# Kernel tuning notes

Measured on AMD Instinct MI355X. Metric: run time of the kernel, lower is better.

## Reference

```python
import jax, jax.numpy as jnp
import numpy as np


def setup_inputs() -> dict:
    key = jax.random.key(0)
    k1, k2 = jax.random.split(key)
    B, K, D = 65536, 4096, 64
    x = jax.random.normal(k1, (B, D), dtype=jnp.float32)
    nodes = jax.random.normal(k2, (K, D), dtype=jnp.float32)  # self.nodes parameter
    return {"x": x, "nodes": nodes}


def reference(x, nodes):
    # torch.cdist(x, nodes, p=2): Euclidean distance matrix [B, K]
    x2 = jnp.sum(x * x, axis=-1, keepdims=True)            # [B, 1]
    n2 = jnp.sum(nodes * nodes, axis=-1)[None, :]          # [1, K]
    d2 = x2 + n2 - 2.0 * (x @ nodes.T)                     # [B, K]
    distances = jnp.sqrt(jnp.maximum(d2, 0.0))
    winning_indices = jnp.argmin(distances, axis=-1)       # [B]
    node_repr = nodes[winning_indices]                     # [B, D] gather
    return node_repr, winning_indices
```

## Files before the change

kernel.cpp:

```cpp
#include <hip/hip_runtime.h>
#include <stdint.h>


typedef unsigned short u16;
typedef __bf16 bf16x8 __attribute__((ext_vector_type(8)));
typedef unsigned short u16x8 __attribute__((ext_vector_type(8)));
typedef float f32x16 __attribute__((ext_vector_type(16)));

#define B_ROWS 65536
#define K_NODES 4096
#define DIM 64
#define CSHIFT 300.0f
#define MERGE_TAU 0.012f

#define OFF_LIST 64
#define OFF_N2F  262208
#define OFF_N2D  278592
#define OFF_BFRAG 311360

__device__ __forceinline__ u16 bf16_rne(float f, float& back) {
    uint32_t u = __float_as_uint(f);
    uint32_t r = u + 0x7FFFu + ((u >> 16) & 1u);
    u16 h = (u16)(r >> 16);
    back = __uint_as_float(((uint32_t)h) << 16);
    return h;
}

__device__ __forceinline__ float pack_tile6(float v, uint32_t t) {
    return __uint_as_float((__float_as_uint(v) & 0xFFFFFFC0u) | t);
}

__global__ __launch_bounds__(256) void prep(const float* __restrict__ nodes,
                                            u16* __restrict__ bfrag,
                                            float* __restrict__ hn2f,
                                            double* __restrict__ n2d,
                                            int* __restrict__ ref_cnt) {
    if (blockIdx.x < 128) {
        int idx = blockIdx.x * 256 + threadIdx.x;
        int t = idx >> 8;
        int rem = idx & 255;
        int l = rem >> 2, c = rem & 3;
        const float* row = nodes + (size_t)(t * 32 + (l & 31)) * DIM + ((l >> 5) * 8);
        float4 f0 = *(const float4*)(row + c * 16);
        float4 f1 = *(const float4*)(row + c * 16 + 4);
        float fs[8] = {-f0.x, -f0.y, -f0.z, -f0.w, -f1.x, -f1.y, -f1.z, -f1.w};
        u16x8 hv, lv;
        #pragma unroll
        for (int j = 0; j < 8; ++j) {
            float hf, dummy;
            u16 hb = bf16_rne(fs[j], hf);
            u16 lb = bf16_rne(fs[j] - hf, dummy);
            hv[j] = hb; lv[j] = lb;
        }
        int base = ((t * 4 + c) * 2) * 512 + l * 8;
        *(u16x8*)(bfrag + base)       = hv;
        *(u16x8*)(bfrag + base + 512) = lv;
    } else {
        if (blockIdx.x == 128 && threadIdx.x == 0) *ref_cnt = 0;
        int k = (blockIdx.x - 128) * 256 + threadIdx.x;
        if (k < K_NODES) {
            const float* r = nodes + (size_t)k * DIM;
            double s = 0.0;
            #pragma unroll
            for (int d = 0; d < DIM; ++d) { double v = (double)r[d]; s += v * v; }
            n2d[k] = s;
            hn2f[k] = CSHIFT + 0.5f * (float)s;
        }
    }
}

__global__ __launch_bounds__(256, 2) void phase1(const float* __restrict__ x,
                                                 const u16* __restrict__ bfrag_g,
                                                 const float* __restrict__ hn2f,
                                                 float* __restrict__ out) {
    const int tid  = threadIdx.x;
    const int lane = tid & 63;
    const int w    = tid >> 6;
    const int col  = lane & 31;
    const int lh   = lane >> 5;
    const int rb   = blockIdx.x >> 1;
    const int h    = blockIdx.x & 1;
    const int rbase = rb * 256 + w * 64;

    bf16x8 ah[2][4], al[2][4];
    #pragma unroll
    for (int t = 0; t < 2; ++t) {
        const float* xp = x + (size_t)(rbase + t * 32 + col) * DIM + lh * 8;
        #pragma unroll
        for (int c = 0; c < 4; ++c) {
            float4 f0 = *(const float4*)(xp + c * 16);
            float4 f1 = *(const float4*)(xp + c * 16 + 4);
            float fs[8] = {f0.x, f0.y, f0.z, f0.w, f1.x, f1.y, f1.z, f1.w};
            u16x8 hv, lv;
            #pragma unroll
            for (int j = 0; j < 8; ++j) {
                float hf, dummy;
                u16 hb = bf16_rne(fs[j], hf);
                u16 lb = bf16_rne(fs[j] - hf, dummy);
                hv[j] = hb; lv[j] = lb;
            }
            union { u16x8 u; bf16x8 b; } cvh, cvl;
            cvh.u = hv; cvl.u = lv;
            ah[t][c] = cvh.b; al[t][c] = cvl.b;
        }
    }

    float b1[2][16], v2[2][16];
    #pragma unroll
    for (int t = 0; t < 2; ++t)
        #pragma unroll
        for (int q = 0; q < 16; ++q) { b1[t][q] = 3.4e38f; v2[t][q] = 3.4e38f; }

    const char* qbase = (const char*)bfrag_g + (size_t)h * 524288 + (size_t)lane * 16;
    const float* hp = hn2f + h * 2048 + col;

    bf16x8 h0, l0, h1, l1, h2, l2, h3, l3;

    #define LD(dsth, dstl, tt, cc) do {                                         \
        const char* _p = qbase + (size_t)(tt) * 8192 + (cc) * 2048;             \
        dsth = *(const bf16x8*)(_p);                                            \
        dstl = *(const bf16x8*)(_p + 1024);                                     \
    } while (0)

    #define MF6(B_h, B_l, cc) do {                                              \
        a0 = __builtin_amdgcn_mfma_f32_32x32x16_bf16(ah[0][cc], B_h, a0, 0, 0, 0); \
        a1 = __builtin_amdgcn_mfma_f32_32x32x16_bf16(ah[1][cc], B_h, a1, 0, 0, 0); \
        a0 = __builtin_amdgcn_mfma_f32_32x32x16_bf16(al[0][cc], B_h, a0, 0, 0, 0); \
        a1 = __builtin_amdgcn_mfma_f32_32x32x16_bf16(al[1][cc], B_h, a1, 0, 0, 0); \
        a0 = __builtin_amdgcn_mfma_f32_32x32x16_bf16(ah[0][cc], B_l, a0, 0, 0, 0); \
        a1 = __builtin_amdgcn_mfma_f32_32x32x16_bf16(ah[1][cc], B_l, a1, 0, 0, 0); \
    } while (0)

    LD(h0, l0, 0, 0);
    LD(h1, l1, 0, 1);
    float hn2_cur = hp[0];

    for (int t = 0; t < 64; ++t) {
        const int tn = (t + 1 < 64) ? t + 1 : 63;
        float hn2_nxt = hp[tn * 32];
        f32x16 a0, a1;
        #pragma unroll
        for (int q = 0; q < 16; ++q) { a0[q] = hn2_cur; a1[q] = hn2_cur; }

        LD(h2, l2, t, 2);
        MF6(h0, l0, 0);
        LD(h3, l3, t, 3);
        MF6(h1, l1, 1);
        LD(h0, l0, tn, 0);
        MF6(h2, l2, 2);
        LD(h1, l1, tn, 1);
        MF6(h3, l3, 3);

        const uint32_t tb = (uint32_t)t;
        #pragma unroll
        for (int q = 0; q < 16; ++q) {
            float p0 = pack_tile6(a0[q], tb);
            v2[0][q] = fminf(v2[0][q], fmaxf(p0, b1[0][q]));
            b1[0][q] = fminf(b1[0][q], p0);
            float p1 = pack_tile6(a1[q], tb);
            v2[1][q] = fminf(v2[1][q], fmaxf(p1, b1[1][q]));
            b1[1][q] = fminf(b1[1][q], p1);
        }
        hn2_cur = hn2_nxt;
    }
    #undef LD
    #undef MF6

    int gi[2][16];
    #pragma unroll
    for (int t = 0; t < 2; ++t)
        #pragma unroll
        for (int q = 0; q < 16; ++q)
            gi[t][q] = (int)(__float_as_uint(b1[t][q]) & 63u) * 32 + col;

    #pragma unroll
    for (int off = 1; off < 32; off <<= 1) {
        #pragma unroll
        for (int t = 0; t < 2; ++t)
            #pragma unroll
            for (int q = 0; q < 16; ++q) {
                float ov  = __shfl_xor(b1[t][q], off, 64);
                float ov2 = __shfl_xor(v2[t][q], off, 64);
                int   og  = __shfl_xor(gi[t][q], off, 64);
                float hi2 = fmaxf(b1[t][q], ov);
                v2[t][q] = fminf(fminf(v2[t][q], ov2), hi2);
                bool take = (ov < b1[t][q]) || (ov == b1[t][q] && og < gi[t][q]);
                b1[t][q] = take ? ov : b1[t][q];
                gi[t][q] = take ? og : gi[t][q];
            }
    }

    if (col == 0) {
        #pragma unroll
        for (int t = 0; t < 2; ++t)
            #pragma unroll
            for (int q = 0; q < 16; ++q) {
                int rloc = (q & 3) + 8 * (q >> 2) + 4 * lh;
                int grow = rb * 256 + w * 64 + t * 32 + rloc;
                float v2p = __uint_as_float((__float_as_uint(v2[t][q]) & 0xFFFFFFE0u)
                                            | (uint32_t)(gi[t][q] & 31));
                *(float2*)(out + (size_t)grow * DIM + h * 2) = make_float2(b1[t][q], v2p);
            }
    }
}

__global__ __launch_bounds__(256) void merge_k(const float* __restrict__ nodes,
                                               float* __restrict__ out,
                                               int* __restrict__ ref_cnt,
                                               int* __restrict__ ref_list) {
    __shared__ int s_win[256];
    const int tid = threadIdx.x;
    const int row = blockIdx.x * 256 + tid;
    float4 cv = *(const float4*)(out + (size_t)row * DIM);
    bool h1w = cv.z < cv.x;
    float wb = h1w ? cv.z : cv.x;
    float lb = h1w ? cv.x : cv.z;
    float v2m = fminf(fminf(cv.y, cv.w), lb);
    uint32_t wbits = __float_as_uint(wb);
    uint32_t vp    = __float_as_uint(h1w ? cv.w : cv.y);
    int gi = (h1w ? 2048 : 0) + (int)(wbits & 63u) * 32 + (int)(vp & 31u);
    out[(size_t)B_ROWS * DIM + row] = (float)gi;
    if (v2m - wb <= MERGE_TAU) {
        int slot = atomicAdd(ref_cnt, 1);
        ref_list[slot] = row;
    }
    s_win[tid] = gi;
    __syncthreads();
    const int base_row = blockIdx.x * 256;
    for (int i = tid; i < 256 * 16; i += 256) {
        int rr = i >> 4, cc = i & 15;
        int wn = s_win[rr];
        float4 v = *(const float4*)(nodes + (size_t)wn * DIM + cc * 4);
        *(float4*)(out + (size_t)(base_row + rr) * DIM + cc * 4) = v;
    }
}

__global__ __launch_bounds__(256) void phase2(const float* __restrict__ x,
                                              const float* __restrict__ nodes,
                                              const double* __restrict__ n2d,
                                              const int* __restrict__ ref_cnt,
                                              const int* __restrict__ ref_list,
                                              float* __restrict__ out) {
    __shared__ double xs[DIM];
    __shared__ double sval[256];
    __shared__ int    sidx[256];
    const int cnt = *ref_cnt;
    for (int li = blockIdx.x; li < cnt; li += gridDim.x) {
        const int row = ref_list[li];
        __syncthreads();
        if (threadIdx.x < DIM) xs[threadIdx.x] = (double)x[(size_t)row * DIM + threadIdx.x];
        __syncthreads();
        double best = 1e300; int bidx = K_NODES;
        for (int k = threadIdx.x; k < K_NODES; k += 256) {
            const float4* np4 = (const float4*)(nodes + (size_t)k * DIM);
            double d0 = 0.0, d1 = 0.0;
            #pragma unroll
            for (int t = 0; t < 16; t += 2) {
                float4 w0 = np4[t], w1 = np4[t + 1];
                d0 += xs[t*4+0]*(double)w0.x + xs[t*4+1]*(double)w0.y
                    + xs[t*4+2]*(double)w0.z + xs[t*4+3]*(double)w0.w;
                d1 += xs[t*4+4]*(double)w1.x + xs[t*4+5]*(double)w1.y
                    + xs[t*4+6]*(double)w1.z + xs[t*4+7]*(double)w1.w;
            }
            double s = n2d[k] - 2.0 * (d0 + d1);
            if (s < best) { best = s; bidx = k; }
        }
        sval[threadIdx.x] = best; sidx[threadIdx.x] = bidx;
        __syncthreads();
        for (int stride = 128; stride > 0; stride >>= 1) {
            if (threadIdx.x < (unsigned)stride) {
                double ov = sval[threadIdx.x + stride];
                int    oi = sidx[threadIdx.x + stride];
                if (ov < sval[threadIdx.x] ||
                    (ov == sval[threadIdx.x] && oi < sidx[threadIdx.x])) {
                    sval[threadIdx.x] = ov; sidx[threadIdx.x] = oi;
                }
            }
            __syncthreads();
        }
        const int wn = sidx[0];
        if (threadIdx.x == 0) out[(size_t)B_ROWS * DIM + row] = (float)wn;
        if (threadIdx.x < 16) {
            float4 v = *(const float4*)(nodes + (size_t)wn * DIM + threadIdx.x * 4);
            *(float4*)(out + (size_t)row * DIM + threadIdx.x * 4) = v;
        }
        __syncthreads();
    }
}

extern "C" void kernel_launch(void* const* d_in, const int* in_sizes, int n_in,
                              void* d_out, int out_size, void* d_ws, size_t ws_size,
                              hipStream_t stream) {
    const float* x     = (const float*)d_in[0];
    const float* nodes = (const float*)d_in[1];
    float* out = (float*)d_out;
    char*  ws  = (char*)d_ws;

    int*    ref_cnt  = (int*)ws;
    int*    ref_list = (int*)(ws + OFF_LIST);
    float*  hn2f     = (float*)(ws + OFF_N2F);
    double* n2d      = (double*)(ws + OFF_N2D);
    u16*    bfrag    = (u16*)(ws + OFF_BFRAG);

    prep<<<144, 256, 0, stream>>>(nodes, bfrag, hn2f, n2d, ref_cnt);
    phase1<<<512, 256, 0, stream>>>(x, bfrag, hn2f, out);
    merge_k<<<B_ROWS / 256, 256, 0, stream>>>(nodes, out, ref_cnt, ref_list);
    phase2<<<1024, 256, 0, stream>>>(x, nodes, n2d, ref_cnt, ref_list, out);
}
```

Before: 205.6 us.

## Split node range into four quarters per block and shrink per-wave row tile

Phase1 now gives each wave 32 rows instead of 64 and splits the 4096 nodes into four quarters of 1024 across blocks, launching 2048 blocks instead of 512. Per-thread accumulators and register state are halved, which is meant to raise occupancy and parallelism, at the cost of reloading node fragments more often per row and doing more cross-lane reductions. The tile index tag shrinks to 5 bits, merge combines four partial results instead of two, and the refinement threshold is lowered so fewer rows go to the exact fp64 pass, which trades some safety margin for less phase2 work.

```diff
diff --git a/kernel.cpp b/kernel.cpp
--- a/kernel.cpp
+++ b/kernel.cpp
@@ -11,7 +11,7 @@
 #define K_NODES 4096
 #define DIM 64
 #define CSHIFT 300.0f
-#define MERGE_TAU 0.012f
+#define MERGE_TAU 0.009f
 
 #define OFF_LIST 64
 #define OFF_N2F  262208
@@ -26,8 +26,8 @@
     return h;
 }
 
-__device__ __forceinline__ float pack_tile6(float v, uint32_t t) {
-    return __uint_as_float((__float_as_uint(v) & 0xFFFFFFC0u) | t);
+__device__ __forceinline__ float pack_tile5(float v, uint32_t t) {
+    return __uint_as_float((__float_as_uint(v) & 0xFFFFFFE0u) | t);
 }
 
 __global__ __launch_bounds__(256) void prep(const float* __restrict__ nodes,
@@ -78,14 +78,13 @@
     const int w    = tid >> 6;
     const int col  = lane & 31;
     const int lh   = lane >> 5;
-    const int rb   = blockIdx.x >> 1;
-    const int h    = blockIdx.x & 1;
-    const int rbase = rb * 256 + w * 64;
-
-    bf16x8 ah[2][4], al[2][4];
-    #pragma unroll
-    for (int t = 0; t < 2; ++t) {
-        const float* xp = x + (size_t)(rbase + t * 32 + col) * DIM + lh * 8;
+    const int rb   = blockIdx.x >> 2;
+    const int qid  = blockIdx.x & 3;
+    const int rbase = rb * 128 + w * 32;
+
+    bf16x8 ah[4], al[4];
+    {
+        const float* xp = x + (size_t)(rbase + col) * DIM + lh * 8;
         #pragma unroll
         for (int c = 0; c < 4; ++c) {
             float4 f0 = *(const float4*)(xp + c * 16);
@@ -101,18 +100,16 @@
             }
             union { u16x8 u; bf16x8 b; } cvh, cvl;
             cvh.u = hv; cvl.u = lv;
-            ah[t][c] = cvh.b; al[t][c] = cvl.b;
-        }
-    }
-
-    float b1[2][16], v2[2][16];
+            ah[c] = cvh.b; al[c] = cvl.b;
+        }
+    }
+
+    float b1[16], v2[16];
     #pragma unroll
-    for (int t = 0; t < 2; ++t)
-        #pragma unroll
-        for (int q = 0; q < 16; ++q) { b1[t][q] = 3.4e38f; v2[t][q] = 3.4e38f; }
-
-    const char* qbase = (const char*)bfrag_g + (size_t)h * 524288 + (size_t)lane * 16;
-    const float* hp = hn2f + h * 2048 + col;
+    for (int q = 0; q < 16; ++q) { b1[q] = 3.4e38f; v2[q] = 3.4e38f; }
+
+    const char* qbase = (const char*)bfrag_g + (size_t)qid * 262144 + (size_t)lane * 16;
+    const float* hp = hn2f + qid * 1024 + col;
 
     bf16x8 h0, l0, h1, l1, h2, l2, h3, l3;
 
@@ -122,85 +119,73 @@
         dstl = *(const bf16x8*)(_p + 1024);                                     \
     } while (0)
 
-    #define MF6(B_h, B_l, cc) do {                                              \
-        a0 = __builtin_amdgcn_mfma_f32_32x32x16_bf16(ah[0][cc], B_h, a0, 0, 0, 0); \
-        a1 = __builtin_amdgcn_mfma_f32_32x32x16_bf16(ah[1][cc], B_h, a1, 0, 0, 0); \
-        a0 = __builtin_amdgcn_mfma_f32_32x32x16_bf16(al[0][cc], B_h, a0, 0, 0, 0); \
-        a1 = __builtin_amdgcn_mfma_f32_32x32x16_bf16(al[1][cc], B_h, a1, 0, 0, 0); \
-        a0 = __builtin_amdgcn_mfma_f32_32x32x16_bf16(ah[0][cc], B_l, a0, 0, 0, 0); \
-        a1 = __builtin_amdgcn_mfma_f32_32x32x16_bf16(ah[1][cc], B_l, a1, 0, 0, 0); \
+    #define MF3(B_h, B_l, cc) do {                                              \
+        a0 = __builtin_amdgcn_mfma_f32_32x32x16_bf16(ah[cc], B_h, a0, 0, 0, 0); \
+        a0 = __builtin_amdgcn_mfma_f32_32x32x16_bf16(al[cc], B_h, a0, 0, 0, 0); \
+        a0 = __builtin_amdgcn_mfma_f32_32x32x16_bf16(ah[cc], B_l, a0, 0, 0, 0); \
     } while (0)
 
     LD(h0, l0, 0, 0);
     LD(h1, l1, 0, 1);
     float hn2_cur = hp[0];
 
-    for (int t = 0; t < 64; ++t) {
-        const int tn = (t + 1 < 64) ? t + 1 : 63;
+    for (int t = 0; t < 32; ++t) {
+        const int tn = (t + 1 < 32) ? t + 1 : 31;
         float hn2_nxt = hp[tn * 32];
-        f32x16 a0, a1;
-        #pragma unroll
-        for (int q = 0; q < 16; ++q) { a0[q] = hn2_cur; a1[q] = hn2_cur; }
+        f32x16 a0;
+        #pragma unroll
+        for (int q = 0; q < 16; ++q) a0[q] = hn2_cur;
 
         LD(h2, l2, t, 2);
-        MF6(h0, l0, 0);
+        MF3(h0, l0, 0);
         LD(h3, l3, t, 3);
-        MF6(h1, l1, 1);
+        MF3(h1, l1, 1);
         LD(h0, l0, tn, 0);
-        MF6(h2, l2, 2);
+        MF3(h2, l2, 2);
         LD(h1, l1, tn, 1);
-        MF6(h3, l3, 3);
+        MF3(h3, l3, 3);
 
         const uint32_t tb = (uint32_t)t;
         #pragma unroll
         for (int q = 0; q < 16; ++q) {
-            float p0 = pack_tile6(a0[q], tb);
-            v2[0][q] = fminf(v2[0][q], fmaxf(p0, b1[0][q]));
-            b1[0][q] = fminf(b1[0][q], p0);
-            float p1 = pack_tile6(a1[q], tb);
-            v2[1][q] = fminf(v2[1][q], fmaxf(p1, b1[1][q]));
-            b1[1][q] = fminf(b1[1][q], p1);
+            float p0 = pack_tile5(a0[q], tb);
+            v2[q] = fminf(v2[q], fmaxf(p0, b1[q]));
+            b1[q] = fminf(b1[q], p0);
         }
         hn2_cur = hn2_nxt;
     }
     #undef LD
-    #undef MF6
-
-    int gi[2][16];
+    #undef MF3
+
+    int gi[16];
     #pragma unroll
-    for (int t = 0; t < 2; ++t)
-        #pragma unroll
-        for (int q = 0; q < 16; ++q)
-            gi[t][q] = (int)(__float_as_uint(b1[t][q]) & 63u) * 32 + col;
+    for (int q = 0; q < 16; ++q)
+        gi[q] = (int)(__float_as_uint(b1[q]) & 31u) * 32 + col;
 
     #pragma unroll
     for (int off = 1; off < 32; off <<= 1) {
         #pragma unroll
-        for (int t = 0; t < 2; ++t)
-            #pragma unroll
-            for (int q = 0; q < 16; ++q) {
-                float ov  = __shfl_xor(b1[t][q], off, 64);
-                float ov2 = __shfl_xor(v2[t][q], off, 64);
-                int   og  = __shfl_xor(gi[t][q], off, 64);
-                float hi2 = fmaxf(b1[t][q], ov);
-                v2[t][q] = fminf(fminf(v2[t][q], ov2), hi2);
-                bool take = (ov < b1[t][q]) || (ov == b1[t][q] && og < gi[t][q]);
-                b1[t][q] = take ? ov : b1[t][q];
-                gi[t][q] = take ? og : gi[t][q];
-            }
+        for (int q = 0; q < 16; ++q) {
+            float ov  = __shfl_xor(b1[q], off, 64);
+            float ov2 = __shfl_xor(v2[q], off, 64);
+            int   og  = __shfl_xor(gi[q], off, 64);
+            float hi2 = fmaxf(b1[q], ov);
+            v2[q] = fminf(fminf(v2[q], ov2), hi2);
+            bool take = (ov < b1[q]) || (ov == b1[q] && og < gi[q]);
+            b1[q] = take ? ov : b1[q];
+            gi[q] = take ? og : gi[q];
+        }
     }
 
     if (col == 0) {
         #pragma unroll
-        for (int t = 0; t < 2; ++t)
-            #pragma unroll
-            for (int q = 0; q < 16; ++q) {
-                int rloc = (q & 3) + 8 * (q >> 2) + 4 * lh;
-                int grow = rb * 256 + w * 64 + t * 32 + rloc;
-                float v2p = __uint_as_float((__float_as_uint(v2[t][q]) & 0xFFFFFFE0u)
-                                            | (uint32_t)(gi[t][q] & 31));
-                *(float2*)(out + (size_t)grow * DIM + h * 2) = make_float2(b1[t][q], v2p);
-            }
+        for (int q = 0; q < 16; ++q) {
+            int rloc = (q & 3) + 8 * (q >> 2) + 4 * lh;
+            int grow = rb * 128 + w * 32 + rloc;
+            float v2p = __uint_as_float((__float_as_uint(v2[q]) & 0xFFFFFFE0u)
+                                        | (uint32_t)(gi[q] & 31));
+            *(float2*)(out + (size_t)grow * DIM + qid * 2) = make_float2(b1[q], v2p);
+        }
     }
 }
 
@@ -211,16 +196,19 @@
     __shared__ int s_win[256];
     const int tid = threadIdx.x;
     const int row = blockIdx.x * 256 + tid;
-    float4 cv = *(const float4*)(out + (size_t)row * DIM);
-    bool h1w = cv.z < cv.x;
-    float wb = h1w ? cv.z : cv.x;
-    float lb = h1w ? cv.x : cv.z;
-    float v2m = fminf(fminf(cv.y, cv.w), lb);
-    uint32_t wbits = __float_as_uint(wb);
-    uint32_t vp    = __float_as_uint(h1w ? cv.w : cv.y);
-    int gi = (h1w ? 2048 : 0) + (int)(wbits & 63u) * 32 + (int)(vp & 31u);
+    float4 cA = *(const float4*)(out + (size_t)row * DIM);
+    float4 cB = *(const float4*)(out + (size_t)row * DIM + 4);
+    float b0 = cA.x, b1 = cA.z, b2 = cB.x, b3 = cB.z;
+    float v0 = cA.y, v1 = cA.w, v2 = cB.y, v3 = cB.w;
+    float wb = b0, vw = v0, sec = 3.4e38f;
+    int qw = 0;
+    if (b1 < wb) { sec = wb; wb = b1; vw = v1; qw = 1; } else sec = fminf(sec, b1);
+    if (b2 < wb) { sec = fminf(sec, wb); wb = b2; vw = v2; qw = 2; } else sec = fminf(sec, b2);
+    if (b3 < wb) { sec = fminf(sec, wb); wb = b3; vw = v3; qw = 3; } else sec = fminf(sec, b3);
+    sec = fminf(fminf(sec, fminf(v0, v1)), fminf(v2, v3));
+    int gi = qw * 1024 + (int)(__float_as_uint(wb) & 31u) * 32 + (int)(__float_as_uint(vw) & 31u);
     out[(size_t)B_ROWS * DIM + row] = (float)gi;
-    if (v2m - wb <= MERGE_TAU) {
+    if (sec - wb <= MERGE_TAU) {
         int slot = atomicAdd(ref_cnt, 1);
         ref_list[slot] = row;
     }
@@ -303,7 +291,7 @@
     u16*    bfrag    = (u16*)(ws + OFF_BFRAG);
 
     prep<<<144, 256, 0, stream>>>(nodes, bfrag, hn2f, n2d, ref_cnt);
-    phase1<<<512, 256, 0, stream>>>(x, bfrag, hn2f, out);
+    phase1<<<2048, 256, 0, stream>>>(x, bfrag, hn2f, out);
     merge_k<<<B_ROWS / 256, 256, 0, stream>>>(nodes, out, ref_cnt, ref_list);
     phase2<<<1024, 256, 0, stream>>>(x, nodes, n2d, ref_cnt, ref_list, out);
 }
```

Result: slower. 264.6 us (+28.7%).

## Split node search into four quarters and batch two rows per refinement block

Applied to the files above, without the earlier changes.

Phase1 now splits the 4096 nodes into four quarters of 32 tiles instead of two halves of 64. This doubles the grid to 1024 blocks and lets the tile index fit in 5 mantissa bits, so the 300 shift is dropped and the merge tolerance is tightened. Each quarter writes its best, second-best and global index into the output scratch, and merge_k reduces the four candidates. Phase2 scores two ambiguous rows per block, so each node load is reused across both rows. The cost is more redundant x conversion per block, extra scratch traffic, and a tighter tolerance that could miss near-ties.

```diff
diff --git a/kernel.cpp b/kernel.cpp
--- a/kernel.cpp
+++ b/kernel.cpp
@@ -10,8 +10,7 @@
 #define B_ROWS 65536
 #define K_NODES 4096
 #define DIM 64
-#define CSHIFT 300.0f
-#define MERGE_TAU 0.012f
+#define MERGE_TAU 0.0065f
 
 #define OFF_LIST 64
 #define OFF_N2F  262208
@@ -26,8 +25,8 @@
     return h;
 }
 
-__device__ __forceinline__ float pack_tile6(float v, uint32_t t) {
-    return __uint_as_float((__float_as_uint(v) & 0xFFFFFFC0u) | t);
+__device__ __forceinline__ float pack_tile5(float v, uint32_t t) {
+    return __uint_as_float((__float_as_uint(v) & 0xFFFFFFE0u) | t);
 }
 
 __global__ __launch_bounds__(256) void prep(const float* __restrict__ nodes,
@@ -64,7 +63,7 @@
             #pragma unroll
             for (int d = 0; d < DIM; ++d) { double v = (double)r[d]; s += v * v; }
             n2d[k] = s;
-            hn2f[k] = CSHIFT + 0.5f * (float)s;
+            hn2f[k] = 0.5f * (float)s;
         }
     }
 }
@@ -78,8 +77,8 @@
     const int w    = tid >> 6;
     const int col  = lane & 31;
     const int lh   = lane >> 5;
-    const int rb   = blockIdx.x >> 1;
-    const int h    = blockIdx.x & 1;
+    const int rb   = blockIdx.x >> 2;
+    const int qid  = blockIdx.x & 3;
     const int rbase = rb * 256 + w * 64;
 
     bf16x8 ah[2][4], al[2][4];
@@ -111,8 +110,8 @@
         #pragma unroll
         for (int q = 0; q < 16; ++q) { b1[t][q] = 3.4e38f; v2[t][q] = 3.4e38f; }
 
-    const char* qbase = (const char*)bfrag_g + (size_t)h * 524288 + (size_t)lane * 16;
-    const float* hp = hn2f + h * 2048 + col;
+    const char* qbase = (const char*)bfrag_g + (size_t)qid * 262144 + (size_t)lane * 16;
+    const float* hp = hn2f + qid * 1024 + col;
 
     bf16x8 h0, l0, h1, l1, h2, l2, h3, l3;
 
@@ -135,8 +134,8 @@
     LD(h1, l1, 0, 1);
     float hn2_cur = hp[0];
 
-    for (int t = 0; t < 64; ++t) {
-        const int tn = (t + 1 < 64) ? t + 1 : 63;
+    for (int t = 0; t < 32; ++t) {
+        const int tn = (t + 1 < 32) ? t + 1 : 31;
         float hn2_nxt = hp[tn * 32];
         f32x16 a0, a1;
         #pragma unroll
@@ -154,10 +153,10 @@
         const uint32_t tb = (uint32_t)t;
         #pragma unroll
         for (int q = 0; q < 16; ++q) {
-            float p0 = pack_tile6(a0[q], tb);
+            float p0 = pack_tile5(a0[q], tb);
             v2[0][q] = fminf(v2[0][q], fmaxf(p0, b1[0][q]));
             b1[0][q] = fminf(b1[0][q], p0);
-            float p1 = pack_tile6(a1[q], tb);
+            float p1 = pack_tile5(a1[q], tb);
             v2[1][q] = fminf(v2[1][q], fmaxf(p1, b1[1][q]));
             b1[1][q] = fminf(b1[1][q], p1);
         }
@@ -171,7 +170,7 @@
     for (int t = 0; t < 2; ++t)
         #pragma unroll
         for (int q = 0; q < 16; ++q)
-            gi[t][q] = (int)(__float_as_uint(b1[t][q]) & 63u) * 32 + col;
+            gi[t][q] = qid * 1024 + (int)(__float_as_uint(b1[t][q]) & 31u) * 32 + col;
 
     #pragma unroll
     for (int off = 1; off < 32; off <<= 1) {
@@ -197,9 +196,8 @@
             for (int q = 0; q < 16; ++q) {
                 int rloc = (q & 3) + 8 * (q >> 2) + 4 * lh;
                 int grow = rb * 256 + w * 64 + t * 32 + rloc;
-                float v2p = __uint_as_float((__float_as_uint(v2[t][q]) & 0xFFFFFFE0u)
-                                            | (uint32_t)(gi[t][q] & 31));
-                *(float2*)(out + (size_t)grow * DIM + h * 2) = make_float2(b1[t][q], v2p);
+                *(float2*)(out + (size_t)grow * DIM + qid * 2) = make_float2(b1[t][q], v2[t][q]);
+                out[(size_t)grow * DIM + 8 + qid] = (float)gi[t][q];
             }
     }
 }
@@ -211,20 +209,27 @@
     __shared__ int s_win[256];
     const int tid = threadIdx.x;
     const int row = blockIdx.x * 256 + tid;
-    float4 cv = *(const float4*)(out + (size_t)row * DIM);
-    bool h1w = cv.z < cv.x;
-    float wb = h1w ? cv.z : cv.x;
-    float lb = h1w ? cv.x : cv.z;
-    float v2m = fminf(fminf(cv.y, cv.w), lb);
-    uint32_t wbits = __float_as_uint(wb);
-    uint32_t vp    = __float_as_uint(h1w ? cv.w : cv.y);
-    int gi = (h1w ? 2048 : 0) + (int)(wbits & 63u) * 32 + (int)(vp & 31u);
-    out[(size_t)B_ROWS * DIM + row] = (float)gi;
-    if (v2m - wb <= MERGE_TAU) {
+    float4 cA = *(const float4*)(out + (size_t)row * DIM);
+    float4 cB = *(const float4*)(out + (size_t)row * DIM + 4);
+    float4 ci = *(const float4*)(out + (size_t)row * DIM + 8);
+    float bv[4] = {cA.x, cA.z, cB.x, cB.z};
+    float vv[4] = {cA.y, cA.w, cB.y, cB.w};
+    int   iv[4] = {(int)ci.x, (int)ci.y, (int)ci.z, (int)ci.w};
+    float wb = bv[0]; int wi = iv[0]; float sec = 3.4e38f;
+    #pragma unroll
+    for (int q = 1; q < 4; ++q) {
+        bool take = (bv[q] < wb) || (bv[q] == wb && iv[q] < wi);
+        sec = fminf(sec, take ? wb : bv[q]);
+        wb = take ? bv[q] : wb;
+        wi = take ? iv[q] : wi;
+    }
+    sec = fminf(fminf(sec, fminf(vv[0], vv[1])), fminf(vv[2], vv[3]));
+    out[(size_t)B_ROWS * DIM + row] = (float)wi;
+    if (sec - wb <= MERGE_TAU) {
         int slot = atomicAdd(ref_cnt, 1);
         ref_list[slot] = row;
     }
-    s_win[tid] = gi;
+    s_win[tid] = wi;
     __syncthreads();
     const int base_row = blockIdx.x * 256;
     for (int i = tid; i < 256 * 16; i += 256) {
@@ -241,50 +246,71 @@
                                               const int* __restrict__ ref_cnt,
                                               const int* __restrict__ ref_list,
                                               float* __restrict__ out) {
-    __shared__ double xs[DIM];
+    __shared__ double xsA[DIM], xsB[DIM];
     __shared__ double sval[256];
     __shared__ int    sidx[256];
+    __shared__ int    rows_s[2];
+    const int tid = threadIdx.x;
     const int cnt = *ref_cnt;
-    for (int li = blockIdx.x; li < cnt; li += gridDim.x) {
-        const int row = ref_list[li];
+    for (int b0 = blockIdx.x * 2; b0 < cnt; b0 += gridDim.x * 2) {
+        const int nr = min(2, cnt - b0);
         __syncthreads();
-        if (threadIdx.x < DIM) xs[threadIdx.x] = (double)x[(size_t)row * DIM + threadIdx.x];
+        if (tid < 2) rows_s[tid] = ref_list[b0 + min(tid, nr - 1)];
         __syncthreads();
-        double best = 1e300; int bidx = K_NODES;
-        for (int k = threadIdx.x; k < K_NODES; k += 256) {
+        if (tid < DIM) {
+            xsA[tid] = (double)x[(size_t)rows_s[0] * DIM + tid];
+            xsB[tid] = (double)x[(size_t)rows_s[1] * DIM + tid];
+        }
+        __syncthreads();
+
+        double bestA = 1e300, bestB = 1e300;
+        int    biA = K_NODES, biB = K_NODES;
+        for (int k = tid; k < K_NODES; k += 256) {
             const float4* np4 = (const float4*)(nodes + (size_t)k * DIM);
-            double d0 = 0.0, d1 = 0.0;
+            double a0 = 0.0, a1 = 0.0, b0d = 0.0, b1d = 0.0;
             #pragma unroll
             for (int t = 0; t < 16; t += 2) {
                 float4 w0 = np4[t], w1 = np4[t + 1];
-                d0 += xs[t*4+0]*(double)w0.x + xs[t*4+1]*(double)w0.y
-                    + xs[t*4+2]*(double)w0.z + xs[t*4+3]*(double)w0.w;
-                d1 += xs[t*4+4]*(double)w1.x + xs[t*4+5]*(double)w1.y
-                    + xs[t*4+6]*(double)w1.z + xs[t*4+7]*(double)w1.w;
-            }
-            double s = n2d[k] - 2.0 * (d0 + d1);
-            if (s < best) { best = s; bidx = k; }
-        }
-        sval[threadIdx.x] = best; sidx[threadIdx.x] = bidx;
-        __syncthreads();
-        for (int stride = 128; stride > 0; stride >>= 1) {
-            if (threadIdx.x < (unsigned)stride) {
-                double ov = sval[threadIdx.x + stride];
-                int    oi = sidx[threadIdx.x + stride];
-                if (ov < sval[threadIdx.x] ||
-                    (ov == sval[threadIdx.x] && oi < sidx[threadIdx.x])) {
-                    sval[threadIdx.x] = ov; sidx[threadIdx.x] = oi;
+                a0 += xsA[t*4+0]*(double)w0.x + xsA[t*4+1]*(double)w0.y
+                    + xsA[t*4+2]*(double)w0.z + xsA[t*4+3]*(double)w0.w;
+                b0d += xsB[t*4+0]*(double)w0.x + xsB[t*4+1]*(double)w0.y
+                     + xsB[t*4+2]*(double)w0.z + xsB[t*4+3]*(double)w0.w;
+                a1 += xsA[t*4+4]*(double)w1.x + xsA[t*4+5]*(double)w1.y
+                    + xsA[t*4+6]*(double)w1.z + xsA[t*4+7]*(double)w1.w;
+                b1d += xsB[t*4+4]*(double)w1.x + xsB[t*4+5]*(double)w1.y
+                     + xsB[t*4+6]*(double)w1.z + xsB[t*4+7]*(double)w1.w;
+            }
+            const double nn = n2d[k];
+            double sA = nn - 2.0 * (a0 + a1);
+            double sB = nn - 2.0 * (b0d + b1d);
+            if (sA < bestA) { bestA = sA; biA = k; }
+            if (sB < bestB) { bestB = sB; biB = k; }
+        }
+
+        #pragma unroll 1
+        for (int r = 0; r < nr; ++r) {
+            sval[tid] = (r == 0) ? bestA : bestB;
+            sidx[tid] = (r == 0) ? biA : biB;
+            __syncthreads();
+            for (int stride = 128; stride > 0; stride >>= 1) {
+                if (tid < (unsigned)stride) {
+                    double ov = sval[tid + stride];
+                    int    oi = sidx[tid + stride];
+                    if (ov < sval[tid] || (ov == sval[tid] && oi < sidx[tid])) {
+                        sval[tid] = ov; sidx[tid] = oi;
+                    }
                 }
+                __syncthreads();
+            }
+            const int wn = sidx[0];
+            const int row = rows_s[r];
+            if (tid == 0) out[(size_t)B_ROWS * DIM + row] = (float)wn;
+            if (tid < 16) {
+                float4 v = *(const float4*)(nodes + (size_t)wn * DIM + tid * 4);
+                *(float4*)(out + (size_t)row * DIM + tid * 4) = v;
             }
             __syncthreads();
         }
-        const int wn = sidx[0];
-        if (threadIdx.x == 0) out[(size_t)B_ROWS * DIM + row] = (float)wn;
-        if (threadIdx.x < 16) {
-            float4 v = *(const float4*)(nodes + (size_t)wn * DIM + threadIdx.x * 4);
-            *(float4*)(out + (size_t)row * DIM + threadIdx.x * 4) = v;
-        }
-        __syncthreads();
     }
 }
 
@@ -303,7 +329,7 @@
     u16*    bfrag    = (u16*)(ws + OFF_BFRAG);
 
     prep<<<144, 256, 0, stream>>>(nodes, bfrag, hn2f, n2d, ref_cnt);
-    phase1<<<512, 256, 0, stream>>>(x, bfrag, hn2f, out);
+    phase1<<<1024, 256, 0, stream>>>(x, bfrag, hn2f, out);
     merge_k<<<B_ROWS / 256, 256, 0, stream>>>(nodes, out, ref_cnt, ref_list);
     phase2<<<1024, 256, 0, stream>>>(x, nodes, n2d, ref_cnt, ref_list, out);
 }
```

Result: no change. 204.2 us (-0.7%).
